# Optimization experiments

Hardware: AMD Instinct MI355X
Metric: run time of the kernel (lower is better)

Reference implementation:

```python
import jax, jax.numpy as jnp
import numpy as np
from jax import lax

BN_EPS = 1e-5


def _conv_block(x, w, b):
    # conv k=3 pad=1 (NCHW), relu, maxpool 2x2 stride 2 (floor)
    y = lax.conv_general_dilated(x, w, (1, 1), [(1, 1), (1, 1)],
                                 dimension_numbers=('NCHW', 'OIHW', 'NCHW'))
    y = jax.nn.relu(y + b[None, :, None, None])
    y = lax.reduce_window(y, -jnp.inf, lax.max, (1, 1, 2, 2), (1, 1, 2, 2), 'VALID')
    return y


def _batchnorm_train(x, g, b):
    # BatchNorm2d in train mode: biased batch stats over (N,H,W)
    m = jnp.mean(x, axis=(0, 2, 3), keepdims=True)
    v = jnp.mean(jnp.square(x - m), axis=(0, 2, 3), keepdims=True)
    return g[None, :, None, None] * (x - m) * lax.rsqrt(v + BN_EPS) + b[None, :, None, None]


def setup_inputs() -> dict:
    key = jax.random.key(0)
    ks = jax.random.split(key, 16)
    B = 4096
    s = lambda k, shape, fan: jax.random.normal(k, shape, jnp.float32) * (1.0 / np.sqrt(fan))
    return {
        'x':   jax.random.normal(ks[0], (B, 1, 28, 28), jnp.float32),
        'cw1': s(ks[1], (32, 1, 3, 3), 9),    'cb1': jnp.zeros((32,), jnp.float32),
        'cw2': s(ks[2], (32, 32, 3, 3), 288), 'cb2': jnp.zeros((32,), jnp.float32),
        'cw3': s(ks[3], (32, 32, 3, 3), 288), 'cb3': jnp.zeros((32,), jnp.float32),
        'bn_g': jnp.ones((32,), jnp.float32), 'bn_b': jnp.zeros((32,), jnp.float32),
        'pw1': s(ks[4], (288, 128), 288), 'pb1': jnp.zeros((128,), jnp.float32),
        'pw2': s(ks[5], (128, 128), 128), 'pb2': jnp.zeros((128,), jnp.float32),
        'pw3': s(ks[6], (128, 3), 128),   'pb3': jnp.zeros((3,), jnp.float32),
        'ew1': s(ks[7], (3, 288, 128), 288), 'eb1': jnp.zeros((3, 128), jnp.float32),
        'ew2': s(ks[8], (3, 128, 128), 128), 'eb2': jnp.zeros((3, 128), jnp.float32),
        'ew3': s(ks[9], (3, 128, 10), 128),  'eb3': jnp.zeros((3, 10), jnp.float32),
    }


def _select_linear(h, oh, ew, eb):
    # per-example expert Linear: compute all 3 tiny experts, pick via one-hot
    y = jnp.einsum('bi,eio->beo', h, ew) + eb[None]  # [B,3,out]
    return jnp.einsum('beo,be->bo', y, oh)


def reference(x, cw1, cb1, cw2, cb2, cw3, cb3, bn_g, bn_b,
              pw1, pb1, pw2, pb2, pw3, pb3,
              ew1, eb1, ew2, eb2, ew3, eb3):
    # conv stack
    y = _conv_block(x, cw1, cb1)
    y = _conv_block(y, cw2, cb2)
    y = _conv_block(y, cw3, cb3)
    y = _batchnorm_train(y, bn_g, bn_b)
    y = y.reshape(y.shape[0], -1)  # [B, 288]

    # ActorCritic approx policy MLP (288 -> 128 -> 128 -> 3), greedy action
    h = jax.nn.relu(y @ pw1 + pb1)
    h = jax.nn.relu(h @ pw2 + pb2)
    logits = h @ pw3 + pb3
    actions = jnp.argmax(logits, axis=-1)          # [B] int, routing decision
    oh = jax.nn.one_hot(actions, 3, dtype=y.dtype)  # [B,3]

    # three SelectionLayers, same per-example routing decision
    y = _select_linear(y, oh, ew1, eb1)
    y = _select_linear(y, oh, ew2, eb2)
    y = _select_linear(y, oh, ew3, eb3)  # [B,10]
    return y, actions
```

## Files before the change

kernel.cpp:

```cpp
#include <hip/hip_runtime.h>

__global__ __launch_bounds__(256) void repack_kernel(
    const float* __restrict__ cw2, const float* __restrict__ cw3,
    float* __restrict__ packed2, float* __restrict__ packed3)
{
    int t = blockIdx.x * 256 + threadIdx.x;
    if (t < 9216) {
        int oc = t & 31, r = t >> 5;
        packed2[t] = cw2[oc * 288 + r];
    } else {
        int t2 = t - 9216;
        int oc = t2 & 31, r = t2 >> 5;
        packed3[t2] = cw3[oc * 288 + r];
    }
}

__global__ __launch_bounds__(256)
void fused_conv_kernel(
    const float* __restrict__ x,
    const float* __restrict__ cw1, const float* __restrict__ cb1,
    const float* __restrict__ packed2, const float* __restrict__ cb2,
    const float* __restrict__ packed3, const float* __restrict__ cb3,
    float* __restrict__ out3)
{
    const int img = blockIdx.x;
    const int tid = threadIdx.x;

    __shared__ float A[1220];
    __shared__ float B[8320];
    __shared__ float b2s[32], b3s[32];

    float* xs1  = A;
    float* w1s  = A + 900;
    float* b1s  = A + 1188;
    float* wck2 = A;
    float* xs2  = B;
    float* sc   = B;
    float* xs3  = B + 1280;
    float* wck3 = B + 4160;
    float* sc2  = B + 5073;

    for (int i = tid; i < 900;  i += 256) xs1[i] = 0.f;
    for (int i = tid; i < 8320; i += 256) B[i] = 0.f;
    __syncthreads();

    for (int i = tid; i < 784; i += 256) {
        int yy = i / 28, xx = i % 28;
        xs1[(yy + 1) * 30 + xx + 1] = x[img * 784 + i];
    }
    for (int i = tid; i < 288; i += 256) {
        int oc = i & 31, tap = i >> 5;
        w1s[i] = cw1[oc * 9 + tap];
    }
    if (tid < 32) { b1s[tid] = cb1[tid]; b2s[tid] = cb2[tid]; b3s[tid] = cb3[tid]; }
    __syncthreads();

    {
        const int c1 = tid & 31;
        float w1r[9];
        #pragma unroll
        for (int t = 0; t < 9; t++) w1r[t] = w1s[t * 32 + c1];
        const float bias1 = b1s[c1];
        for (int o = tid; o < 32 * 196; o += 256) {
            int p = o >> 5;
            int py = p / 14, px = p % 14;
            int base = (2 * py) * 30 + 2 * px;
            float P[16];
            #pragma unroll
            for (int r = 0; r < 4; r++) {
                float2 u0 = *(const float2*)&xs1[base + r * 30];
                float2 u1 = *(const float2*)&xs1[base + r * 30 + 2];
                P[r * 4 + 0] = u0.x; P[r * 4 + 1] = u0.y;
                P[r * 4 + 2] = u1.x; P[r * 4 + 3] = u1.y;
            }
            float a00 = 0.f, a01 = 0.f, a10 = 0.f, a11 = 0.f;
            #pragma unroll
            for (int ky = 0; ky < 3; ky++)
                #pragma unroll
                for (int kx = 0; kx < 3; kx++) {
                    float w = w1r[ky * 3 + kx];
                    a00 = fmaf(P[ky * 4 + kx],           w, a00);
                    a01 = fmaf(P[ky * 4 + kx + 1],       w, a01);
                    a10 = fmaf(P[(ky + 1) * 4 + kx],     w, a10);
                    a11 = fmaf(P[(ky + 1) * 4 + kx + 1], w, a11);
                }
            float v = fmaxf(fmaxf(fmaxf(a00, a01), fmaxf(a10, a11)) + bias1, 0.f);
            int r = py + 1, col = px + 1;
            xs2[c1 * 260 + r * 16 + ((((col >> 2) + r) & 3) << 2) + (col & 3)] = v;
        }
    }

    const int g  = tid >> 7;
    const int u  = tid & 127;
    const int cb = u & 7, R = u >> 3;
    const int oc0 = cb * 4;
    const bool act2 = (u < 112);

    float acc[4][14];
    #pragma unroll
    for (int a = 0; a < 4; a++)
        #pragma unroll
        for (int c = 0; c < 14; c++) acc[a][c] = 0.f;

    float pf[5];
    #pragma unroll
    for (int k = 0; k < 5; k++) {
        int idx = tid + k * 256;
        pf[k] = (idx < 1152) ? packed2[idx] : 0.f;
    }

    for (int ch = 0; ch < 8; ch++) {
        __syncthreads();
        #pragma unroll
        for (int k = 0; k < 5; k++) {
            int idx = tid + k * 256;
            if (idx < 1152) wck2[idx] = pf[k];
        }
        if (ch < 7) {
            #pragma unroll
            for (int k = 0; k < 5; k++) {
                int idx = tid + k * 256;
                pf[k] = (idx < 1152) ? packed2[(ch + 1) * 1152 + idx] : 0.f;
            }
        }
        __syncthreads();
        if (act2) {
            #pragma unroll
            for (int d = 0; d < 2; d++) {
                const int ld = g * 2 + d;
                const int ic = ch * 4 + ld;
                const float* wd = &wck2[ld * 288 + oc0];
                const int pb = ic * 260;
                #pragma unroll
                for (int ky = 0; ky < 3; ky++) {
                    const int rp = R + ky;
                    const int rb = pb + rp * 16;
                    float row[16];
                    #pragma unroll
                    for (int q = 0; q < 4; q++) {
                        const float4 t = *(const float4*)&xs2[rb + (((q + rp) & 3) << 2)];
                        row[q * 4 + 0] = t.x; row[q * 4 + 1] = t.y;
                        row[q * 4 + 2] = t.z; row[q * 4 + 3] = t.w;
                    }
                    const float4 wa = *(const float4*)&wd[(ky * 3 + 0) * 32];
                    const float4 wb = *(const float4*)&wd[(ky * 3 + 1) * 32];
                    const float4 wc = *(const float4*)&wd[(ky * 3 + 2) * 32];
                    #pragma unroll
                    for (int c = 0; c < 14; c++) {
                        acc[0][c] = fmaf(row[c],     wa.x, acc[0][c]);
                        acc[1][c] = fmaf(row[c],     wa.y, acc[1][c]);
                        acc[2][c] = fmaf(row[c],     wa.z, acc[2][c]);
                        acc[3][c] = fmaf(row[c],     wa.w, acc[3][c]);
                        acc[0][c] = fmaf(row[c + 1], wb.x, acc[0][c]);
                        acc[1][c] = fmaf(row[c + 1], wb.y, acc[1][c]);
                        acc[2][c] = fmaf(row[c + 1], wb.z, acc[2][c]);
                        acc[3][c] = fmaf(row[c + 1], wb.w, acc[3][c]);
                        acc[0][c] = fmaf(row[c + 2], wc.x, acc[0][c]);
                        acc[1][c] = fmaf(row[c + 2], wc.y, acc[1][c]);
                        acc[2][c] = fmaf(row[c + 2], wc.z, acc[2][c]);
                        acc[3][c] = fmaf(row[c + 2], wc.w, acc[3][c]);
                    }
                }
            }
        }
    }

    __syncthreads();
    if (g == 1 && act2) {
        #pragma unroll
        for (int a = 0; a < 4; a++)
            #pragma unroll
            for (int c = 0; c < 14; c++) sc[u * 57 + a * 14 + c] = acc[a][c];
    }
    __syncthreads();
    if (g == 0 && act2) {
        #pragma unroll
        for (int a = 0; a < 4; a++)
            #pragma unroll
            for (int c = 0; c < 14; c++) acc[a][c] += sc[u * 57 + a * 14 + c];
    }
    __syncthreads();

    for (int i = tid; i < 2880; i += 256) xs3[i] = 0.f;
    float hm[4][7];
    if (g == 0 && act2) {
        #pragma unroll
        for (int a = 0; a < 4; a++)
            #pragma unroll
            for (int c = 0; c < 7; c++)
                hm[a][c] = fmaxf(acc[a][2 * c], acc[a][2 * c + 1]);
        if (R & 1) {
            #pragma unroll
            for (int a = 0; a < 4; a++)
                #pragma unroll
                for (int c = 0; c < 7; c++) sc2[u * 29 + a * 7 + c] = hm[a][c];
        }
    }
    __syncthreads();
    if (g == 0 && act2 && !(R & 1)) {
        const int py = R >> 1;
        #pragma unroll
        for (int a = 0; a < 4; a++)
            #pragma unroll
            for (int c = 0; c < 7; c++) {
                float v = fmaxf(hm[a][c], sc2[(u + 8) * 29 + a * 7 + c]);
                v = fmaxf(v + b2s[oc0 + a], 0.f);
                xs3[(oc0 + a) * 90 + (py + 1) * 10 + (c + 1)] = v;
            }
    }

    const int u3 = tid & 127;
    const bool act3 = (u3 < 72);
    const int cq3 = u3 & 7, pos = u3 >> 3;
    const int oc30 = cq3 * 4;
    const int py3 = pos / 3, px3 = pos % 3;
    const int base3 = (2 * py3) * 10 + 2 * px3;

    float a3[4][4];
    #pragma unroll
    for (int a = 0; a < 4; a++)
        #pragma unroll
        for (int q = 0; q < 4; q++) a3[a][q] = 0.f;

    float pg[9];
    #pragma unroll
    for (int k = 0; k < 9; k++) pg[k] = packed3[tid + k * 256];

    for (int ch = 0; ch < 4; ch++) {
        __syncthreads();
        #pragma unroll
        for (int k = 0; k < 9; k++) wck3[tid + k * 256] = pg[k];
        if (ch < 3) {
            #pragma unroll
            for (int k = 0; k < 9; k++) pg[k] = packed3[(ch + 1) * 2304 + tid + k * 256];
        }
        __syncthreads();
        if (act3) {
            #pragma unroll 2
            for (int d = 0; d < 4; d++) {
                const int ld = g * 4 + d;
                const int ic = ch * 8 + ld;
                const float* xp = &xs3[ic * 90 + base3];
                float P[16];
                #pragma unroll
                for (int r = 0; r < 4; r++) {
                    float2 u0 = *(const float2*)&xp[r * 10];
                    float2 u1 = *(const float2*)&xp[r * 10 + 2];
                    P[r * 4 + 0] = u0.x; P[r * 4 + 1] = u0.y;
                    P[r * 4 + 2] = u1.x; P[r * 4 + 3] = u1.y;
                }
                const float* wd = &wck3[ld * 288 + oc30];
                #pragma unroll
                for (int tap = 0; tap < 9; tap++) {
                    const int ky = tap / 3, kx = tap % 3;
                    const float4 wv = *(const float4*)&wd[tap * 32];
                    const float x00 = P[ky * 4 + kx];
                    const float x01 = P[ky * 4 + kx + 1];
                    const float x10 = P[(ky + 1) * 4 + kx];
                    const float x11 = P[(ky + 1) * 4 + kx + 1];
                    a3[0][0] = fmaf(x00, wv.x, a3[0][0]); a3[0][1] = fmaf(x01, wv.x, a3[0][1]);
                    a3[0][2] = fmaf(x10, wv.x, a3[0][2]); a3[0][3] = fmaf(x11, wv.x, a3[0][3]);
                    a3[1][0] = fmaf(x00, wv.y, a3[1][0]); a3[1][1] = fmaf(x01, wv.y, a3[1][1]);
                    a3[1][2] = fmaf(x10, wv.y, a3[1][2]); a3[1][3] = fmaf(x11, wv.y, a3[1][3]);
                    a3[2][0] = fmaf(x00, wv.z, a3[2][0]); a3[2][1] = fmaf(x01, wv.z, a3[2][1]);
                    a3[2][2] = fmaf(x10, wv.z, a3[2][2]); a3[2][3] = fmaf(x11, wv.z, a3[2][3]);
                    a3[3][0] = fmaf(x00, wv.w, a3[3][0]); a3[3][1] = fmaf(x01, wv.w, a3[3][1]);
                    a3[3][2] = fmaf(x10, wv.w, a3[3][2]); a3[3][3] = fmaf(x11, wv.w, a3[3][3]);
                }
            }
        }
    }

    __syncthreads();
    if (g == 1 && act3) {
        #pragma unroll
        for (int a = 0; a < 4; a++)
            #pragma unroll
            for (int q = 0; q < 4; q++) sc[u3 * 17 + a * 4 + q] = a3[a][q];
    }
    __syncthreads();
    if (g == 0 && act3) {
        #pragma unroll
        for (int a = 0; a < 4; a++)
            #pragma unroll
            for (int q = 0; q < 4; q++) a3[a][q] += sc[u3 * 17 + a * 4 + q];
        float4 res;
        float* r = (float*)&res;
        #pragma unroll
        for (int a = 0; a < 4; a++) {
            float v = fmaxf(fmaxf(a3[a][0], a3[a][1]), fmaxf(a3[a][2], a3[a][3]));
            r[a] = fmaxf(v + b3s[oc30 + a], 0.f);
        }
        *(float4*)&out3[img * 288 + pos * 32 + oc30] = res;
    }
}

__global__ __launch_bounds__(256) void bn_part_kernel(
    const float* __restrict__ out3, float* __restrict__ pS, float* __restrict__ pSS)
{
    const int blk = blockIdx.x;
    const int c = threadIdx.x & 31, ml = threadIdx.x >> 5;
    float s = 0.f, ss = 0.f;
    const int base = blk * 576 + ml;
    for (int k = 0; k < 72; k++) {
        float v = out3[(base + k * 8) * 32 + c];
        s += v; ss = fmaf(v, v, ss);
    }
    __shared__ float rs[256], rss[256];
    rs[threadIdx.x] = s; rss[threadIdx.x] = ss;
    __syncthreads();
    if (threadIdx.x < 32) {
        float S = 0.f, SS = 0.f;
        #pragma unroll
        for (int m = 0; m < 8; m++) { S += rs[threadIdx.x + 32 * m]; SS += rss[threadIdx.x + 32 * m]; }
        pS[blk * 32 + threadIdx.x] = S;
        pSS[blk * 32 + threadIdx.x] = SS;
    }
}

__global__ __launch_bounds__(64) void bn_final_kernel(
    const float* __restrict__ pS, const float* __restrict__ pSS,
    const float* __restrict__ bng, const float* __restrict__ bnb,
    float* __restrict__ stats)
{
    int c = threadIdx.x;
    if (c < 32) {
        float S = 0.f, SS = 0.f;
        for (int b = 0; b < 64; b++) { S += pS[b * 32 + c]; SS += pSS[b * 32 + c]; }
        const float inv_n = 1.f / (4096.f * 9.f);
        float mean = S * inv_n;
        float var = SS * inv_n - mean * mean;
        float a = bng[c] * rsqrtf(var + 1e-5f);
        stats[c] = a;
        stats[32 + c] = bnb[c] - a * mean;
    }
}

__global__ __launch_bounds__(256) void mlp_select_kernel(
    const float* __restrict__ out3, const float* __restrict__ stats,
    const float* __restrict__ pw1, const float* __restrict__ pb1,
    const float* __restrict__ pw2, const float* __restrict__ pb2,
    const float* __restrict__ pw3, const float* __restrict__ pb3,
    const float* __restrict__ ew1, const float* __restrict__ eb1,
    const float* __restrict__ ew2, const float* __restrict__ eb2,
    const float* __restrict__ ew3, const float* __restrict__ eb3,
    float* __restrict__ out)
{
    const int tid = threadIdx.x;
    const int img0 = blockIdx.x * 8;

    __shared__ float ysT[288 * 14];
    __shared__ float hAT[128 * 14];
    __shared__ float hBT[128 * 14];
    __shared__ float lg[24];
    __shared__ int   acts[8];
    __shared__ float sa[32], sb[32];

    if (tid < 32) { sa[tid] = stats[tid]; sb[tid] = stats[32 + tid]; }
    __syncthreads();

    for (int it = 0; it < 3; it++) {
        int i4 = it * 256 + tid;
        if (i4 < 576) {
            int e = i4 / 72, jq = i4 - e * 72;
            float4 v = *(const float4*)&out3[(img0 + e) * 288 + jq * 4];
            int j = jq * 4;
            ysT[(j + 0) * 14 + e] = fmaf(sa[(j + 0) & 31], v.x, sb[(j + 0) & 31]);
            ysT[(j + 1) * 14 + e] = fmaf(sa[(j + 1) & 31], v.y, sb[(j + 1) & 31]);
            ysT[(j + 2) * 14 + e] = fmaf(sa[(j + 2) & 31], v.z, sb[(j + 2) & 31]);
            ysT[(j + 3) * 14 + e] = fmaf(sa[(j + 3) & 31], v.w, sb[(j + 3) & 31]);
        }
    }
    __syncthreads();

    const int n2 = tid & 63, eT = tid >> 6, e0 = eT * 2;
    float acc[2][2];

    #pragma unroll
    for (int e = 0; e < 2; e++) { acc[e][0] = pb1[n2 * 2]; acc[e][1] = pb1[n2 * 2 + 1]; }
    for (int k = 0; k < 288; k++) {
        int i = (k & 31) * 9 + (k >> 5);
        float2 w = *(const float2*)&pw1[i * 128 + n2 * 2];
        float2 yv = *(const float2*)&ysT[k * 14 + e0];
        acc[0][0] = fmaf(yv.x, w.x, acc[0][0]); acc[0][1] = fmaf(yv.x, w.y, acc[0][1]);
        acc[1][0] = fmaf(yv.y, w.x, acc[1][0]); acc[1][1] = fmaf(yv.y, w.y, acc[1][1]);
    }
    #pragma unroll
    for (int e = 0; e < 2; e++)
        #pragma unroll
        for (int d = 0; d < 2; d++)
            hAT[(n2 * 2 + d) * 14 + e0 + e] = fmaxf(acc[e][d], 0.f);
    __syncthreads();

    #pragma unroll
    for (int e = 0; e < 2; e++) { acc[e][0] = pb2[n2 * 2]; acc[e][1] = pb2[n2 * 2 + 1]; }
    for (int k = 0; k < 128; k++) {
        float2 w = *(const float2*)&pw2[k * 128 + n2 * 2];
        float2 hv = *(const float2*)&hAT[k * 14 + e0];
        acc[0][0] = fmaf(hv.x, w.x, acc[0][0]); acc[0][1] = fmaf(hv.x, w.y, acc[0][1]);
        acc[1][0] = fmaf(hv.y, w.x, acc[1][0]); acc[1][1] = fmaf(hv.y, w.y, acc[1][1]);
    }
    #pragma unroll
    for (int e = 0; e < 2; e++)
        #pragma unroll
        for (int d = 0; d < 2; d++)
            hBT[(n2 * 2 + d) * 14 + e0 + e] = fmaxf(acc[e][d], 0.f);
    __syncthreads();

    if (tid < 24) {
        int e = tid / 3, o = tid - e * 3;
        float s = pb3[o];
        for (int k = 0; k < 128; k++) s = fmaf(hBT[k * 14 + e], pw3[k * 3 + o], s);
        lg[e * 3 + o] = s;
    }
    __syncthreads();
    if (tid < 8) {
        float l0 = lg[tid * 3], l1 = lg[tid * 3 + 1], l2 = lg[tid * 3 + 2];
        int a = 0; float best = l0;
        if (l1 > best) { best = l1; a = 1; }
        if (l2 > best) { best = l2; a = 2; }
        acts[tid] = a;
        out[4096 * 10 + img0 + tid] = (float)a;
    }
    __syncthreads();

    const int a0 = acts[e0], a1 = acts[e0 + 1];

    {
        const float* wb0 = ew1 + a0 * 36864;
        const float* wb1 = ew1 + a1 * 36864;
        #pragma unroll
        for (int e = 0; e < 2; e++) { acc[e][0] = 0.f; acc[e][1] = 0.f; }
        for (int k = 0; k < 288; k++) {
            int i = (k & 31) * 9 + (k >> 5);
            float2 wA = *(const float2*)&wb0[i * 128 + n2 * 2];
            float2 wB = *(const float2*)&wb1[i * 128 + n2 * 2];
            float2 yv = *(const float2*)&ysT[k * 14 + e0];
            acc[0][0] = fmaf(yv.x, wA.x, acc[0][0]); acc[0][1] = fmaf(yv.x, wA.y, acc[0][1]);
            acc[1][0] = fmaf(yv.y, wB.x, acc[1][0]); acc[1][1] = fmaf(yv.y, wB.y, acc[1][1]);
        }
        hAT[(n2 * 2 + 0) * 14 + e0 + 0] = acc[0][0] + eb1[a0 * 128 + n2 * 2 + 0];
        hAT[(n2 * 2 + 1) * 14 + e0 + 0] = acc[0][1] + eb1[a0 * 128 + n2 * 2 + 1];
        hAT[(n2 * 2 + 0) * 14 + e0 + 1] = acc[1][0] + eb1[a1 * 128 + n2 * 2 + 0];
        hAT[(n2 * 2 + 1) * 14 + e0 + 1] = acc[1][1] + eb1[a1 * 128 + n2 * 2 + 1];
    }
    __syncthreads();

    {
        const float* wb0 = ew2 + a0 * 16384;
        const float* wb1 = ew2 + a1 * 16384;
        #pragma unroll
        for (int e = 0; e < 2; e++) { acc[e][0] = 0.f; acc[e][1] = 0.f; }
        for (int k = 0; k < 128; k++) {
            float2 wA = *(const float2*)&wb0[k * 128 + n2 * 2];
            float2 wB = *(const float2*)&wb1[k * 128 + n2 * 2];
            float2 hv = *(const float2*)&hAT[k * 14 + e0];
            acc[0][0] = fmaf(hv.x, wA.x, acc[0][0]); acc[0][1] = fmaf(hv.x, wA.y, acc[0][1]);
            acc[1][0] = fmaf(hv.y, wB.x, acc[1][0]); acc[1][1] = fmaf(hv.y, wB.y, acc[1][1]);
        }
        hBT[(n2 * 2 + 0) * 14 + e0 + 0] = acc[0][0] + eb2[a0 * 128 + n2 * 2 + 0];
        hBT[(n2 * 2 + 1) * 14 + e0 + 0] = acc[0][1] + eb2[a0 * 128 + n2 * 2 + 1];
        hBT[(n2 * 2 + 0) * 14 + e0 + 1] = acc[1][0] + eb2[a1 * 128 + n2 * 2 + 0];
        hBT[(n2 * 2 + 1) * 14 + e0 + 1] = acc[1][1] + eb2[a1 * 128 + n2 * 2 + 1];
    }
    __syncthreads();

    if (tid < 80) {
        int e = tid / 10, o = tid - e * 10;
        int a = acts[e];
        float s = eb3[a * 10 + o];
        const float* w3 = &ew3[a * 1280];
        for (int k = 0; k < 128; k++) s = fmaf(hBT[k * 14 + e], w3[k * 10 + o], s);
        out[(img0 + e) * 10 + o] = s;
    }
}

extern "C" void kernel_launch(void* const* d_in, const int* in_sizes, int n_in,
                              void* d_out, int out_size, void* d_ws, size_t ws_size,
                              hipStream_t stream)
{
    const float* x   = (const float*)d_in[0];
    const float* cw1 = (const float*)d_in[1];
    const float* cb1 = (const float*)d_in[2];
    const float* cw2 = (const float*)d_in[3];
    const float* cb2 = (const float*)d_in[4];
    const float* cw3 = (const float*)d_in[5];
    const float* cb3 = (const float*)d_in[6];
    const float* bng = (const float*)d_in[7];
    const float* bnb = (const float*)d_in[8];
    const float* pw1 = (const float*)d_in[9];
    const float* pb1 = (const float*)d_in[10];
    const float* pw2 = (const float*)d_in[11];
    const float* pb2 = (const float*)d_in[12];
    const float* pw3 = (const float*)d_in[13];
    const float* pb3 = (const float*)d_in[14];
    const float* ew1 = (const float*)d_in[15];
    const float* eb1 = (const float*)d_in[16];
    const float* ew2 = (const float*)d_in[17];
    const float* eb2 = (const float*)d_in[18];
    const float* ew3 = (const float*)d_in[19];
    const float* eb3 = (const float*)d_in[20];

    float* out     = (float*)d_out;
    float* out3    = (float*)d_ws;
    float* pS      = out3 + 4096 * 288;
    float* pSS     = pS + 2048;
    float* stats   = pSS + 2048;
    float* packed2 = stats + 64;
    float* packed3 = packed2 + 9216;

    repack_kernel<<<72, 256, 0, stream>>>(cw2, cw3, packed2, packed3);
    fused_conv_kernel<<<4096, 256, 0, stream>>>(x, cw1, cb1, packed2, cb2, packed3, cb3, out3);
    bn_part_kernel<<<64, 256, 0, stream>>>(out3, pS, pSS);
    bn_final_kernel<<<1, 64, 0, stream>>>(pS, pSS, bng, bnb, stats);
    mlp_select_kernel<<<512, 256, 0, stream>>>(out3, stats,
                                               pw1, pb1, pw2, pb2, pw3, pb3,
                                               ew1, eb1, ew2, eb2, ew3, eb3, out);
}
```

Before: 453.4 us.

## Fuse BN statistics into conv kernel via atomics; remap MLP threads per example

```diff
diff --git a/kernel.cpp b/kernel.cpp
--- a/kernel.cpp
+++ b/kernel.cpp
@@ -21,7 +21,7 @@
     const float* __restrict__ cw1, const float* __restrict__ cb1,
     const float* __restrict__ packed2, const float* __restrict__ cb2,
     const float* __restrict__ packed3, const float* __restrict__ cb3,
-    float* __restrict__ out3)
+    float* __restrict__ out3, float* __restrict__ gstats)
 {
     const int img = blockIdx.x;
     const int tid = threadIdx.x;
@@ -279,54 +279,52 @@
             for (int q = 0; q < 4; q++) sc[u3 * 17 + a * 4 + q] = a3[a][q];
     }
     __syncthreads();
-    if (g == 0 && act3) {
+    float rres[4];
+    const bool writer = (g == 0 && act3);
+    if (writer) {
         #pragma unroll
         for (int a = 0; a < 4; a++)
             #pragma unroll
             for (int q = 0; q < 4; q++) a3[a][q] += sc[u3 * 17 + a * 4 + q];
         float4 res;
-        float* r = (float*)&res;
         #pragma unroll
         for (int a = 0; a < 4; a++) {
             float v = fmaxf(fmaxf(a3[a][0], a3[a][1]), fmaxf(a3[a][2], a3[a][3]));
-            r[a] = fmaxf(v + b3s[oc30 + a], 0.f);
-        }
+            rres[a] = fmaxf(v + b3s[oc30 + a], 0.f);
+        }
+        res.x = rres[0]; res.y = rres[1]; res.z = rres[2]; res.w = rres[3];
         *(float4*)&out3[img * 288 + pos * 32 + oc30] = res;
     }
+
+    __syncthreads();
+    for (int i = tid; i < 576; i += 256) B[i] = 0.f;
+    __syncthreads();
+    if (writer) {
+        #pragma unroll
+        for (int a = 0; a < 4; a++) {
+            B[pos * 64 + oc30 + a]      = rres[a];
+            B[pos * 64 + 32 + oc30 + a] = rres[a] * rres[a];
+        }
+    }
+    __syncthreads();
+    if (tid < 64) {
+        int c = tid & 31, part = tid >> 5;
+        float s = 0.f;
+        #pragma unroll
+        for (int p = 0; p < 9; p++) s += B[p * 64 + part * 32 + c];
+        atomicAdd(&gstats[part * 32 + c], s);
+    }
 }
 
-__global__ __launch_bounds__(256) void bn_part_kernel(
-    const float* __restrict__ out3, float* __restrict__ pS, float* __restrict__ pSS)
-{
-    const int blk = blockIdx.x;
-    const int c = threadIdx.x & 31, ml = threadIdx.x >> 5;
-    float s = 0.f, ss = 0.f;
-    const int base = blk * 576 + ml;
-    for (int k = 0; k < 72; k++) {
-        float v = out3[(base + k * 8) * 32 + c];
-        s += v; ss = fmaf(v, v, ss);
-    }
-    __shared__ float rs[256], rss[256];
-    rs[threadIdx.x] = s; rss[threadIdx.x] = ss;
-    __syncthreads();
-    if (threadIdx.x < 32) {
-        float S = 0.f, SS = 0.f;
-        #pragma unroll
-        for (int m = 0; m < 8; m++) { S += rs[threadIdx.x + 32 * m]; SS += rss[threadIdx.x + 32 * m]; }
-        pS[blk * 32 + threadIdx.x] = S;
-        pSS[blk * 32 + threadIdx.x] = SS;
-    }
-}
-
 __global__ __launch_bounds__(64) void bn_final_kernel(
-    const float* __restrict__ pS, const float* __restrict__ pSS,
+    const float* __restrict__ gstats,
     const float* __restrict__ bng, const float* __restrict__ bnb,
     float* __restrict__ stats)
 {
     int c = threadIdx.x;
     if (c < 32) {
-        float S = 0.f, SS = 0.f;
-        for (int b = 0; b < 64; b++) { S += pS[b * 32 + c]; SS += pSS[b * 32 + c]; }
+        float S = gstats[c];
+        float SS = gstats[32 + c];
         const float inv_n = 1.f / (4096.f * 9.f);
         float mean = S * inv_n;
         float var = SS * inv_n - mean * mean;
@@ -373,38 +371,39 @@
     }
     __syncthreads();
 
-    const int n2 = tid & 63, eT = tid >> 6, e0 = eT * 2;
-    float acc[2][2];
-
-    #pragma unroll
-    for (int e = 0; e < 2; e++) { acc[e][0] = pb1[n2 * 2]; acc[e][1] = pb1[n2 * 2 + 1]; }
-    for (int k = 0; k < 288; k++) {
-        int i = (k & 31) * 9 + (k >> 5);
-        float2 w = *(const float2*)&pw1[i * 128 + n2 * 2];
-        float2 yv = *(const float2*)&ysT[k * 14 + e0];
-        acc[0][0] = fmaf(yv.x, w.x, acc[0][0]); acc[0][1] = fmaf(yv.x, w.y, acc[0][1]);
-        acc[1][0] = fmaf(yv.y, w.x, acc[1][0]); acc[1][1] = fmaf(yv.y, w.y, acc[1][1]);
-    }
-    #pragma unroll
-    for (int e = 0; e < 2; e++)
-        #pragma unroll
-        for (int d = 0; d < 2; d++)
-            hAT[(n2 * 2 + d) * 14 + e0 + e] = fmaxf(acc[e][d], 0.f);
-    __syncthreads();
-
-    #pragma unroll
-    for (int e = 0; e < 2; e++) { acc[e][0] = pb2[n2 * 2]; acc[e][1] = pb2[n2 * 2 + 1]; }
-    for (int k = 0; k < 128; k++) {
-        float2 w = *(const float2*)&pw2[k * 128 + n2 * 2];
-        float2 hv = *(const float2*)&hAT[k * 14 + e0];
-        acc[0][0] = fmaf(hv.x, w.x, acc[0][0]); acc[0][1] = fmaf(hv.x, w.y, acc[0][1]);
-        acc[1][0] = fmaf(hv.y, w.x, acc[1][0]); acc[1][1] = fmaf(hv.y, w.y, acc[1][1]);
-    }
-    #pragma unroll
-    for (int e = 0; e < 2; e++)
-        #pragma unroll
-        for (int d = 0; d < 2; d++)
-            hBT[(n2 * 2 + d) * 14 + e0 + e] = fmaxf(acc[e][d], 0.f);
+    const int n4 = tid & 31;
+    const int eE = tid >> 5;
+    float acc[4];
+
+    {
+        float4 b = *(const float4*)&pb1[n4 * 4];
+        acc[0] = b.x; acc[1] = b.y; acc[2] = b.z; acc[3] = b.w;
+        for (int k = 0; k < 288; k++) {
+            int i = (k & 31) * 9 + (k >> 5);
+            float4 w = *(const float4*)&pw1[i * 128 + n4 * 4];
+            float yv = ysT[k * 14 + eE];
+            acc[0] = fmaf(yv, w.x, acc[0]); acc[1] = fmaf(yv, w.y, acc[1]);
+            acc[2] = fmaf(yv, w.z, acc[2]); acc[3] = fmaf(yv, w.w, acc[3]);
+        }
+        #pragma unroll
+        for (int j = 0; j < 4; j++)
+            hAT[(n4 * 4 + j) * 14 + eE] = fmaxf(acc[j], 0.f);
+    }
+    __syncthreads();
+
+    {
+        float4 b = *(const float4*)&pb2[n4 * 4];
+        acc[0] = b.x; acc[1] = b.y; acc[2] = b.z; acc[3] = b.w;
+        for (int k = 0; k < 128; k++) {
+            float4 w = *(const float4*)&pw2[k * 128 + n4 * 4];
+            float hv = hAT[k * 14 + eE];
+            acc[0] = fmaf(hv, w.x, acc[0]); acc[1] = fmaf(hv, w.y, acc[1]);
+            acc[2] = fmaf(hv, w.z, acc[2]); acc[3] = fmaf(hv, w.w, acc[3]);
+        }
+        #pragma unroll
+        for (int j = 0; j < 4; j++)
+            hBT[(n4 * 4 + j) * 14 + eE] = fmaxf(acc[j], 0.f);
+    }
     __syncthreads();
 
     if (tid < 24) {
@@ -424,52 +423,48 @@
     }
     __syncthreads();
 
-    const int a0 = acts[e0], a1 = acts[e0 + 1];
+    const int a = acts[eE];
 
     {
-        const float* wb0 = ew1 + a0 * 36864;
-        const float* wb1 = ew1 + a1 * 36864;
-        #pragma unroll
-        for (int e = 0; e < 2; e++) { acc[e][0] = 0.f; acc[e][1] = 0.f; }
+        const float* wb = ew1 + a * 36864;
+        acc[0] = 0.f; acc[1] = 0.f; acc[2] = 0.f; acc[3] = 0.f;
         for (int k = 0; k < 288; k++) {
             int i = (k & 31) * 9 + (k >> 5);
-            float2 wA = *(const float2*)&wb0[i * 128 + n2 * 2];
-            float2 wB = *(const float2*)&wb1[i * 128 + n2 * 2];
-            float2 yv = *(const float2*)&ysT[k * 14 + e0];
-            acc[0][0] = fmaf(yv.x, wA.x, acc[0][0]); acc[0][1] = fmaf(yv.x, wA.y, acc[0][1]);
-            acc[1][0] = fmaf(yv.y, wB.x, acc[1][0]); acc[1][1] = fmaf(yv.y, wB.y, acc[1][1]);
-        }
-        hAT[(n2 * 2 + 0) * 14 + e0 + 0] = acc[0][0] + eb1[a0 * 128 + n2 * 2 + 0];
-        hAT[(n2 * 2 + 1) * 14 + e0 + 0] = acc[0][1] + eb1[a0 * 128 + n2 * 2 + 1];
-        hAT[(n2 * 2 + 0) * 14 + e0 + 1] = acc[1][0] + eb1[a1 * 128 + n2 * 2 + 0];
-        hAT[(n2 * 2 + 1) * 14 + e0 + 1] = acc[1][1] + eb1[a1 * 128 + n2 * 2 + 1];
+            float4 w = *(const float4*)&wb[i * 128 + n4 * 4];
+            float yv = ysT[k * 14 + eE];
+            acc[0] = fmaf(yv, w.x, acc[0]); acc[1] = fmaf(yv, w.y, acc[1]);
+            acc[2] = fmaf(yv, w.z, acc[2]); acc[3] = fmaf(yv, w.w, acc[3]);
+        }
+        float4 b = *(const float4*)&eb1[a * 128 + n4 * 4];
+        hAT[(n4 * 4 + 0) * 14 + eE] = acc[0] + b.x;
+        hAT[(n4 * 4 + 1) * 14 + eE] = acc[1] + b.y;
+        hAT[(n4 * 4 + 2) * 14 + eE] = acc[2] + b.z;
+        hAT[(n4 * 4 + 3) * 14 + eE] = acc[3] + b.w;
     }
     __syncthreads();
 
     {
-        const float* wb0 = ew2 + a0 * 16384;
-        const float* wb1 = ew2 + a1 * 16384;
-        #pragma unroll
-        for (int e = 0; e < 2; e++) { acc[e][0] = 0.f; acc[e][1] = 0.f; }
+        const float* wb = ew2 + a * 16384;
+        acc[0] = 0.f; acc[1] = 0.f; acc[2] = 0.f; acc[3] = 0.f;
         for (int k = 0; k < 128; k++) {
-            float2 wA = *(const float2*)&wb0[k * 128 + n2 * 2];
-            float2 wB = *(const float2*)&wb1[k * 128 + n2 * 2];
-            float2 hv = *(const float2*)&hAT[k * 14 + e0];
-            acc[0][0] = fmaf(hv.x, wA.x, acc[0][0]); acc[0][1] = fmaf(hv.x, wA.y, acc[0][1]);
-            acc[1][0] = fmaf(hv.y, wB.x, acc[1][0]); acc[1][1] = fmaf(hv.y, wB.y, acc[1][1]);
-        }
-        hBT[(n2 * 2 + 0) * 14 + e0 + 0] = acc[0][0] + eb2[a0 * 128 + n2 * 2 + 0];
-        hBT[(n2 * 2 + 1) * 14 + e0 + 0] = acc[0][1] + eb2[a0 * 128 + n2 * 2 + 1];
-        hBT[(n2 * 2 + 0) * 14 + e0 + 1] = acc[1][0] + eb2[a1 * 128 + n2 * 2 + 0];
-        hBT[(n2 * 2 + 1) * 14 + e0 + 1] = acc[1][1] + eb2[a1 * 128 + n2 * 2 + 1];
+            float4 w = *(const float4*)&wb[k * 128 + n4 * 4];
+            float hv = hAT[k * 14 + eE];
+            acc[0] = fmaf(hv, w.x, acc[0]); acc[1] = fmaf(hv, w.y, acc[1]);
+            acc[2] = fmaf(hv, w.z, acc[2]); acc[3] = fmaf(hv, w.w, acc[3]);
+        }
+        float4 b = *(const float4*)&eb2[a * 128 + n4 * 4];
+        hBT[(n4 * 4 + 0) * 14 + eE] = acc[0] + b.x;
+        hBT[(n4 * 4 + 1) * 14 + eE] = acc[1] + b.y;
+        hBT[(n4 * 4 + 2) * 14 + eE] = acc[2] + b.z;
+        hBT[(n4 * 4 + 3) * 14 + eE] = acc[3] + b.w;
     }
     __syncthreads();
 
     if (tid < 80) {
         int e = tid / 10, o = tid - e * 10;
-        int a = acts[e];
-        float s = eb3[a * 10 + o];
-        const float* w3 = &ew3[a * 1280];
+        int aa = acts[e];
+        float s = eb3[aa * 10 + o];
+        const float* w3 = &ew3[aa * 1280];
         for (int k = 0; k < 128; k++) s = fmaf(hBT[k * 14 + e], w3[k * 10 + o], s);
         out[(img0 + e) * 10 + o] = s;
     }
@@ -503,16 +498,16 @@
 
     float* out     = (float*)d_out;
     float* out3    = (float*)d_ws;
-    float* pS      = out3 + 4096 * 288;
-    float* pSS     = pS + 2048;
-    float* stats   = pSS + 2048;
+    float* gstats  = out3 + 4096 * 288;
+    float* stats   = gstats + 64;
     float* packed2 = stats + 64;
     float* packed3 = packed2 + 9216;
 
+    hipMemsetAsync(gstats, 0, 64 * sizeof(float), stream);
     repack_kernel<<<72, 256, 0, stream>>>(cw2, cw3, packed2, packed3);
-    fused_conv_kernel<<<4096, 256, 0, stream>>>(x, cw1, cb1, packed2, cb2, packed3, cb3, out3);
-    bn_part_kernel<<<64, 256, 0, stream>>>(out3, pS, pSS);
-    bn_final_kernel<<<1, 64, 0, stream>>>(pS, pSS, bng, bnb, stats);
+    fused_conv_kernel<<<4096, 256, 0, stream>>>(x, cw1, cb1, packed2, cb2,
+                                                packed3, cb3, out3, gstats);
+    bn_final_kernel<<<1, 64, 0, stream>>>(gstats, bng, bnb, stats);
     mlp_select_kernel<<<512, 256, 0, stream>>>(out3, stats,
                                                pw1, pb1, pw2, pb2, pw3, pb3,
                                                ew1, eb1, ew2, eb2, ew3, eb3, out);
```

Result: faster. 424.8 us (-6.3%).
